# Kernel tuning notes

Measured on AMD Instinct MI355X. Metric: run time of the kernel, lower is better.

## Reference

```python
import jax, jax.numpy as jnp
import numpy as np

IMG_SIZE = 500
FM = 31
RATIOS = [1.0, 2.0, 0.5]
SCALES = [128, 256, 512]
PRE_NMS_TOPN = 6000
POST_NMS_TOPN = 1500
IOU_THRESHOLD = 0.7
VARIANCES = (0.1, 0.1, 0.2, 0.2)
BATCH = 64
TOTAL_ANCHORS = FM * FM * len(RATIOS) * len(SCALES)  # 8649


def generate_anchors():
    # normalized [y1, x1, y2, x2] anchors on a FM x FM grid
    stride = 1.0 / FM
    ctr = (np.arange(FM, dtype=np.float32) + 0.5) * stride
    cx, cy = np.meshgrid(ctr, ctr)
    centers = np.stack([cy.ravel(), cx.ravel()], axis=-1)  # [FM*FM, 2] (cy, cx)
    hs, ws = [], []
    for scale in SCALES:
        for ratio in RATIOS:
            ws.append((scale * np.sqrt(ratio)) / IMG_SIZE)
            hs.append((scale / np.sqrt(ratio)) / IMG_SIZE)
    hw = np.stack([np.array(hs, np.float32), np.array(ws, np.float32)], axis=-1)  # [9, 2]
    mins = centers[:, None, :] - hw[None] / 2.0
    maxs = centers[:, None, :] + hw[None] / 2.0
    boxes = np.concatenate([mins, maxs], axis=-1).reshape(-1, 4)  # [A, 4]
    return np.clip(boxes, 0.0, 1.0).astype(np.float32)


def delta_to_bbox(anchors, deltas):
    # anchors: [A,4], deltas: [B,A,4] (dy, dx, dh, dw) -> [B,A,4] (y1,x1,y2,x2)
    anc_h = anchors[:, 2] - anchors[:, 0]
    anc_w = anchors[:, 3] - anchors[:, 1]
    anc_cy = anchors[:, 0] + 0.5 * anc_h
    anc_cx = anchors[:, 1] + 0.5 * anc_w
    h = jnp.exp(deltas[..., 2]) * anc_h
    w = jnp.exp(deltas[..., 3]) * anc_w
    cy = deltas[..., 0] * anc_h + anc_cy
    cx = deltas[..., 1] * anc_w + anc_cx
    return jnp.stack([cy - 0.5 * h, cx - 0.5 * w, cy + 0.5 * h, cx + 0.5 * w], axis=-1)


def pairwise_iou_one_vs_all(sel_box, boxes):
    # sel_box: [B,1,4], boxes: [B,N,4] -> iou [B,N]
    y1 = jnp.maximum(sel_box[..., 0], boxes[..., 0])
    x1 = jnp.maximum(sel_box[..., 1], boxes[..., 1])
    y2 = jnp.minimum(sel_box[..., 2], boxes[..., 2])
    x2 = jnp.minimum(sel_box[..., 3], boxes[..., 3])
    inter = jnp.maximum(y2 - y1, 0.0) * jnp.maximum(x2 - x1, 0.0)
    area_s = (sel_box[..., 2] - sel_box[..., 0]) * (sel_box[..., 3] - sel_box[..., 1])
    area_b = (boxes[..., 2] - boxes[..., 0]) * (boxes[..., 3] - boxes[..., 1])
    return inter / (area_s + area_b - inter + 1e-9)


def batched_greedy_nms(boxes, scores, max_out, iou_threshold):
    # boxes [B,N,4], scores [B,N]; greedy NMS, vectorized over batch, scan over picks
    B, N, _ = boxes.shape

    def step(active, _):
        masked = jnp.where(active, scores, -jnp.inf)            # [B,N]
        idx = jnp.argmax(masked, axis=1)                         # [B]
        sel_score = jnp.take_along_axis(masked, idx[:, None], axis=1)[:, 0]
        sel_box = jnp.take_along_axis(boxes, idx[:, None, None], axis=1)  # [B,1,4]
        iou = pairwise_iou_one_vs_all(sel_box, boxes)            # [B,N]
        active = active & (iou <= iou_threshold)
        valid = jnp.isfinite(sel_score)
        out_box = jnp.where(valid[:, None], sel_box[:, 0, :], 0.0)
        out_score = jnp.where(valid, sel_score, 0.0)
        return active, (out_box, out_score)

    active0 = jnp.ones((B, N), dtype=bool)
    _, (out_boxes, out_scores) = jax.lax.scan(step, active0, None, length=max_out)
    out_boxes = jnp.transpose(out_boxes, (1, 0, 2))   # [B,max_out,4]
    out_scores = jnp.transpose(out_scores, (1, 0))    # [B,max_out]
    # tf.image.combined_non_max_suppression clips output boxes to [0,1] by default
    return jnp.clip(out_boxes, 0.0, 1.0), out_scores


def setup_inputs() -> dict:
    key = jax.random.key(0)
    k1, k2, k3 = jax.random.split(key, 3)
    rpn_bbox_deltas = jax.random.normal(k1, (BATCH, FM, FM, 36), dtype=jnp.float32)
    rpn_probs = jax.random.uniform(k2, (BATCH, FM, FM, 9), dtype=jnp.float32)
    gt_labels = jax.random.randint(k3, (BATCH, 10), 0, 20).astype(jnp.int64)
    anchors = jnp.asarray(generate_anchors())
    return {"rpn_bbox_deltas": rpn_bbox_deltas, "rpn_probs": rpn_probs,
            "gt_labels": gt_labels, "anchors": anchors}


def reference(rpn_bbox_deltas, rpn_probs, gt_labels, anchors):
    B = rpn_bbox_deltas.shape[0]
    A = anchors.shape[0]
    variances = jnp.asarray(VARIANCES, dtype=rpn_bbox_deltas.dtype)
    deltas = rpn_bbox_deltas.reshape(B, A, 4) * variances
    probs = rpn_probs.reshape(B, A)
    rpn_bboxes = delta_to_bbox(anchors, deltas)              # [B,A,4]
    top_scores, top_idx = jax.lax.top_k(probs, PRE_NMS_TOPN)  # sorted desc
    top_boxes = jnp.take_along_axis(rpn_bboxes, top_idx[:, :, None], axis=1)
    roi_bboxes, roi_scores = batched_greedy_nms(top_boxes, top_scores,
                                                POST_NMS_TOPN, IOU_THRESHOLD)
    return roi_bboxes, roi_scores
```

## Files before the change

kernel.cpp:

```cpp
#include <hip/hip_runtime.h>
#include <math.h>

typedef unsigned int u32;
typedef unsigned short u16;
typedef unsigned long long u64;

#define BATCH 64
#define A_TOT 8649
#define TOPN  6000
#define POST  1500
#define NB    4096
#define NT    512
#define NWAVE 8
#define NSLOT 12
#define NCHUNK 94
#define DONEBIT 0x80000000u
#define CNTMASK 0x7FFFFFFFu
#define GUARD_MAX (1 << 18)

#define LDS_BYTES 106496

__global__ __launch_bounds__(NT, 2) void roibbox_kernel(
    const float* __restrict__ deltas,
    const float* __restrict__ probs,
    const float* __restrict__ anchors,
    float* __restrict__ out)
{
    #pragma clang fp contract(off)
    __shared__ alignas(16) char smem[LDS_BYTES];
    u64*    keysL   = (u64*)   (smem + 0);
    u32*    bucketA = (u32*)   (smem + 69632);
    u32*    bucketB = (u32*)   (smem + 86016);
    u32*    stemp   = (u32*)   (smem + 102400);
    float4* ringL   = (float4*)(smem + 69632);
    u16*    ppL     = (u16*)   (smem + 93632);
    u32*    ctrlP   = (u32*)   (smem + 105632);
    u32*    ctrlF   = (u32*)   (smem + 105636);
    u32*    bmL     = (u32*)   (smem + 105640);

    const int tid = threadIdx.x;
    const int b   = blockIdx.x;
    const u32 lane = (u32)tid & 63u;
    const u32 w    = (u32)tid >> 6;
    const float* pb = probs + (size_t)b * A_TOT;

    #pragma unroll
    for (int i = 0; i < NB/NT; ++i) bucketA[tid + i*NT] = 0u;
    __syncthreads();

    for (int j = tid; j < A_TOT; j += NT) {
        float s = pb[j];
        int bkt = (int)(s * (float)NB);
        bkt = (NB-1) - min(max(bkt, 0), NB-1);
        atomicAdd(&bucketA[bkt], 1u);
    }
    __syncthreads();

    {
        int base8 = tid << 3;
        u32 c[8]; u32 ms = 0;
        #pragma unroll
        for (int i = 0; i < 8; ++i) { c[i] = bucketA[base8+i]; ms += c[i]; }
        stemp[tid] = ms;
        __syncthreads();
        int src = 0;
        for (int off = 1; off < NT; off <<= 1) {
            u32 v = stemp[src*NT + tid];
            if (tid >= off) v += stemp[src*NT + tid - off];
            stemp[(src^1)*NT + tid] = v;
            __syncthreads();
            src ^= 1;
        }
        u32 excl = stemp[src*NT + tid] - ms;
        #pragma unroll
        for (int i = 0; i < 8; ++i) {
            bucketA[base8+i] = excl; bucketB[base8+i] = excl; excl += c[i];
        }
    }
    __syncthreads();

    for (int j = tid; j < A_TOT; j += NT) {
        float s = pb[j];
        int bkt = (int)(s * (float)NB);
        bkt = (NB-1) - min(max(bkt, 0), NB-1);
        u32 pos = atomicAdd(&bucketB[bkt], 1u);
        keysL[pos] = ((u64)__float_as_uint(s) << 32) | (u64)(~(u32)j);
    }
    __syncthreads();

    for (int bkt = tid; bkt < NB; bkt += NT) {
        int begin = (int)bucketA[bkt], end = (int)bucketB[bkt];
        for (int k = begin + 1; k < end; ++k) {
            u64 key = keysL[k];
            int m = k - 1;
            while (m >= begin && keysL[m] < key) { keysL[m+1] = keysL[m]; --m; }
            keysL[m+1] = key;
        }
    }
    __syncthreads();

    float ry1[NSLOT], rx1[NSLOT], ry2[NSLOT], rx2[NSLOT], rA[NSLOT];
    u32 mask = 0;
    #pragma unroll
    for (int i = 0; i < NSLOT; ++i) {
        u32 s = (u32)i*8u + w;
        u32 r = s*64u + lane;
        ry1[i]=0.f; rx1[i]=0.f; ry2[i]=0.f; rx2[i]=0.f; rA[i]=0.f;
        if (s < NCHUNK && r < TOPN) {
            u64 k = keysL[r];
            u32 aidx = ~((u32)k);
            float4 av = *(const float4*)(anchors + (size_t)aidx * 4);
            float4 dv = *(const float4*)(deltas + ((size_t)b * A_TOT + aidx) * 4);
            float d0 = dv.x*0.1f, d1 = dv.y*0.1f, d2 = dv.z*0.2f, d3 = dv.w*0.2f;
            float ah = av.z - av.x, aw = av.w - av.y;
            float acy = av.x + 0.5f*ah, acx = av.y + 0.5f*aw;
            float h  = (float)exp((double)d2) * ah;
            float wd = (float)exp((double)d3) * aw;
            float cy = d0*ah + acy;
            float cx = d1*aw + acx;
            ry1[i] = cy - 0.5f*h;  rx1[i] = cx - 0.5f*wd;
            ry2[i] = cy + 0.5f*h;  rx2[i] = cx + 0.5f*wd;
            rA[i]  = (ry2[i]-ry1[i])*(rx2[i]-rx1[i]);
            mask |= 1u << i;
        }
    }
    u32 slotAlive = 0;
    #pragma unroll
    for (int i = 0; i < NSLOT; ++i)
        if (__ballot((mask >> i) & 1u)) slotAlive |= 1u << i;

    for (int j = tid; j < TOPN/2; j += NT) ((u32*)ppL)[j] = 0xFFFFFFFFu;
    if (tid == 0) { *ctrlP = 0u; *ctrlF = 0u; bmL[0] = 0u; bmL[1] = 0u; bmL[2] = 0xC0000000u; }
    __syncthreads();

    const double MTHR = (double)0.7f + 0x1p-25;

    auto scanNext = [&](u32 from) -> u32 {
        for (u32 k = from >> 5; k < 3u; ++k) {
            u32 v = ~__hip_atomic_load(&bmL[k], __ATOMIC_RELAXED, __HIP_MEMORY_SCOPE_WORKGROUP);
            if (k == (from >> 5)) v &= ~((1u << (from & 31u)) - 1u);
            if (v) return k*32u + (u32)__builtin_ctz(v);
        }
        return 96u;
    };

    u32 consumed = 0;
    for (int g = 0; g < GUARD_MAX; ++g) {
        u32 pv = __hip_atomic_load(ctrlP, __ATOMIC_ACQUIRE, __HIP_MEMORY_SCOPE_WORKGROUP);
        if (pv & DONEBIT) break;
        u32 cnt = pv & CNTMASK;

        if (cnt > consumed) {
            if (slotAlive) {
                float4 e = ringL[consumed];
                for (u32 q = consumed; q < cnt; ++q) {
                    float4 en = e;
                    if (q + 1 < cnt) en = ringL[q + 1];
                    float sA = (e.z - e.x) * (e.w - e.y);
                    #pragma unroll
                    for (int i = 0; i < NSLOT; ++i) {
                        if (slotAlive & (1u << i)) {
                            float yy1 = fmaxf(e.x, ry1[i]);
                            float xx1 = fmaxf(e.y, rx1[i]);
                            float yy2 = fminf(e.z, ry2[i]);
                            float xx2 = fminf(e.w, rx2[i]);
                            float inter = fmaxf(yy2 - yy1, 0.f) * fmaxf(xx2 - xx1, 0.f);
                            float den = ((sA + rA[i]) - inter) + 1e-9f;
                            if ((double)inter >= MTHR * (double)den) mask &= ~(1u << i);
                        }
                    }
                    e = en;
                }
                u32 na = 0;
                #pragma unroll
                for (int i = 0; i < NSLOT; ++i)
                    if ((slotAlive >> i) & 1u)
                        if (__ballot((mask >> i) & 1u)) na |= 1u << i;
                u32 died = slotAlive & ~na;
                slotAlive = na;
                if (died && lane == 0) {
                    #pragma unroll
                    for (int i = 0; i < NSLOT; ++i)
                        if ((died >> i) & 1u) {
                            u32 s = (u32)i*8u + w;
                            __hip_atomic_fetch_or(&bmL[s >> 5], 1u << (s & 31u),
                                                  __ATOMIC_RELAXED, __HIP_MEMORY_SCOPE_WORKGROUP);
                        }
                }
            }
            consumed = cnt;
            continue;
        }

        u32 f = __hip_atomic_load(ctrlF, __ATOMIC_ACQUIRE, __HIP_MEMORY_SCOPE_WORKGROUP);
        if ((f & 7u) == w) {
            u32 pv2 = __hip_atomic_load(ctrlP, __ATOMIC_ACQUIRE, __HIP_MEMORY_SCOPE_WORKGROUP);
            if (pv2 & DONEBIT) break;
            u32 cnt2 = pv2 & CNTMASK;
            if (cnt2 != consumed) continue;
            u32 fi = f >> 3;
            if ((slotAlive >> fi) & 1u) {
                float cy1, cx1, cy2, cx2, cA_;
                switch (fi) {
                    case 0:  cy1=ry1[0];  cx1=rx1[0];  cy2=ry2[0];  cx2=rx2[0];  cA_=rA[0];  break;
                    case 1:  cy1=ry1[1];  cx1=rx1[1];  cy2=ry2[1];  cx2=rx2[1];  cA_=rA[1];  break;
                    case 2:  cy1=ry1[2];  cx1=rx1[2];  cy2=ry2[2];  cx2=rx2[2];  cA_=rA[2];  break;
                    case 3:  cy1=ry1[3];  cx1=rx1[3];  cy2=ry2[3];  cx2=rx2[3];  cA_=rA[3];  break;
                    case 4:  cy1=ry1[4];  cx1=rx1[4];  cy2=ry2[4];  cx2=rx2[4];  cA_=rA[4];  break;
                    case 5:  cy1=ry1[5];  cx1=rx1[5];  cy2=ry2[5];  cx2=rx2[5];  cA_=rA[5];  break;
                    case 6:  cy1=ry1[6];  cx1=rx1[6];  cy2=ry2[6];  cx2=rx2[6];  cA_=rA[6];  break;
                    case 7:  cy1=ry1[7];  cx1=rx1[7];  cy2=ry2[7];  cx2=rx2[7];  cA_=rA[7];  break;
                    case 8:  cy1=ry1[8];  cx1=rx1[8];  cy2=ry2[8];  cx2=rx2[8];  cA_=rA[8];  break;
                    case 9:  cy1=ry1[9];  cx1=rx1[9];  cy2=ry2[9];  cx2=rx2[9];  cA_=rA[9];  break;
                    case 10: cy1=ry1[10]; cx1=rx1[10]; cy2=ry2[10]; cx2=rx2[10]; cA_=rA[10]; break;
                    default: cy1=ry1[11]; cx1=rx1[11]; cy2=ry2[11]; cx2=rx2[11]; cA_=rA[11]; break;
                }
                u64 am = __ballot((mask >> fi) & 1u);
                mask &= ~(1u << fi);
                slotAlive &= ~(1u << fi);
                u32 pc = cnt2;
                bool alldone = false;
                __builtin_amdgcn_s_setprio(1);
                while (true) {
                    if (!am) {
                        if (lane == 0)
                            __hip_atomic_fetch_or(&bmL[f >> 5], 1u << (f & 31u),
                                                  __ATOMIC_RELAXED, __HIP_MEMORY_SCOPE_WORKGROUP);
                        u32 nxt = scanNext(f + 1u);
                        if (nxt >= NCHUNK) {
                            if (lane == 0)
                                __hip_atomic_store(ctrlP, pc | DONEBIT, __ATOMIC_RELEASE,
                                                   __HIP_MEMORY_SCOPE_WORKGROUP);
                            alldone = true;
                        } else if (lane == 0) {
                            __hip_atomic_store(ctrlF, nxt, __ATOMIC_RELEASE,
                                               __HIP_MEMORY_SCOPE_WORKGROUP);
                        }
                        break;
                    }
                    u32 ol = (u32)__builtin_ctzll(am);
                    float sy1 = __uint_as_float((u32)__builtin_amdgcn_readlane((int)__float_as_uint(cy1), (int)ol));
                    float sx1 = __uint_as_float((u32)__builtin_amdgcn_readlane((int)__float_as_uint(cx1), (int)ol));
                    float sy2 = __uint_as_float((u32)__builtin_amdgcn_readlane((int)__float_as_uint(cy2), (int)ol));
                    float sx2 = __uint_as_float((u32)__builtin_amdgcn_readlane((int)__float_as_uint(cx2), (int)ol));
                    if (lane == ol) {
                        ppL[f*64u + ol] = (u16)pc;
                        ringL[pc] = make_float4(cy1, cx1, cy2, cx2);
                    }
                    float sA = (sy2 - sy1) * (sx2 - sx1);
                    float yy1 = fmaxf(sy1, cy1);
                    float xx1 = fmaxf(sx1, cx1);
                    float yy2 = fminf(sy2, cy2);
                    float xx2 = fminf(sx2, cx2);
                    float inter = fmaxf(yy2 - yy1, 0.f) * fmaxf(xx2 - xx1, 0.f);
                    float den = ((sA + cA_) - inter) + 1e-9f;
                    u64 supp = __ballot((double)inter >= MTHR * (double)den);
                    am &= ~supp;
                    ++pc;
                    u32 val = pc | ((pc >= POST) ? DONEBIT : 0u);
                    if (lane == 0)
                        __hip_atomic_store(ctrlP, val, __ATOMIC_RELEASE,
                                           __HIP_MEMORY_SCOPE_WORKGROUP);
                    if (pc >= POST) { alldone = true; break; }
                }
                __builtin_amdgcn_s_setprio(0);
                if (alldone) break;
                continue;
            } else {
                if (lane == 0)
                    __hip_atomic_fetch_or(&bmL[f >> 5], 1u << (f & 31u),
                                          __ATOMIC_RELAXED, __HIP_MEMORY_SCOPE_WORKGROUP);
                u32 nxt = scanNext(f + 1u);
                if (nxt >= NCHUNK) {
                    if (lane == 0)
                        __hip_atomic_store(ctrlP, cnt2 | DONEBIT, __ATOMIC_RELEASE,
                                           __HIP_MEMORY_SCOPE_WORKGROUP);
                    break;
                }
                if (lane == 0)
                    __hip_atomic_store(ctrlF, nxt, __ATOMIC_RELEASE,
                                       __HIP_MEMORY_SCOPE_WORKGROUP);
                continue;
            }
        }
        __builtin_amdgcn_s_sleep(1);
    }
    __syncthreads();
    u32 pend = (*ctrlP) & CNTMASK;

    const size_t sbase = (size_t)BATCH * POST * 4;
    #pragma unroll
    for (int i = 0; i < NSLOT; ++i) {
        u32 s = (u32)i*8u + w;
        u32 r = s*64u + lane;
        if (s < NCHUNK && r < TOPN) {
            u32 v = (u32)ppL[r];
            if (v != 0xFFFFu) {
                size_t row = (size_t)b * POST + v;
                float* ob = out + row * 4;
                ob[0] = fminf(fmaxf(ry1[i], 0.f), 1.f);
                ob[1] = fminf(fmaxf(rx1[i], 0.f), 1.f);
                ob[2] = fminf(fmaxf(ry2[i], 0.f), 1.f);
                ob[3] = fminf(fmaxf(rx2[i], 0.f), 1.f);
                out[sbase + row] = __uint_as_float((u32)(keysL[r] >> 32));
            }
        }
    }
    for (int p = (int)pend + tid; p < POST; p += NT) {
        size_t row = (size_t)b * POST + p;
        float* ob = out + row * 4;
        ob[0]=0.f; ob[1]=0.f; ob[2]=0.f; ob[3]=0.f;
        out[sbase + row] = 0.f;
    }
}

extern "C" void kernel_launch(void* const* d_in, const int* in_sizes, int n_in,
                              void* d_out, int out_size, void* d_ws, size_t ws_size,
                              hipStream_t stream) {
    const float* deltas  = (const float*)d_in[0];
    const float* probs   = (const float*)d_in[1];
    const float* anchors = (const float*)d_in[3];
    float* out = (float*)d_out;

    roibbox_kernel<<<dim3(BATCH), dim3(NT), 0, stream>>>(deltas, probs, anchors, out);
}
```

Before: 1.368 ms.

## Lazily apply suppression only to slots near the NMS frontier, with fp32 fast-path threshold

Each wave now tracks how far each register slot has been checked against the kept-box ring, and only applies new kept boxes to slots within a horizon of the current frontier chunk. Far-away slots catch up later, which lets them drop out early without testing every kept box, and avoids per-step IoU work on chunks that are still far from the frontier. The IoU comparison first uses fp32 bounds and falls back to the exact double check only when a lane is near the threshold. This adds bookkeeping and catch-up loops and makes the control flow more complex; the frontier wave must wait until its slot is fully caught up.

```diff
diff --git a/kernel.cpp b/kernel.cpp
--- a/kernel.cpp
+++ b/kernel.cpp
@@ -14,6 +14,7 @@
 #define NWAVE 8
 #define NSLOT 12
 #define NCHUNK 94
+#define HOR   12
 #define DONEBIT 0x80000000u
 #define CNTMASK 0x7FFFFFFFu
 #define GUARD_MAX (1 << 18)
@@ -129,6 +130,10 @@
     for (int i = 0; i < NSLOT; ++i)
         if (__ballot((mask >> i) & 1u)) slotAlive |= 1u << i;
 
+    u32 consS[NSLOT];
+    #pragma unroll
+    for (int i = 0; i < NSLOT; ++i) consS[i] = 0u;
+
     for (int j = tid; j < TOPN/2; j += NT) ((u32*)ppL)[j] = 0xFFFFFFFFu;
     if (tid == 0) { *ctrlP = 0u; *ctrlF = 0u; bmL[0] = 0u; bmL[1] = 0u; bmL[2] = 0xC0000000u; }
     __syncthreads();
@@ -144,62 +149,110 @@
         return 96u;
     };
 
-    u32 consumed = 0;
+    #define APPLY(i, e, sA)  do {                                              \
+        float yy1 = fmaxf((e).x, ry1[i]);                                      \
+        float xx1 = fmaxf((e).y, rx1[i]);                                      \
+        float yy2 = fminf((e).z, ry2[i]);                                      \
+        float xx2 = fminf((e).w, rx2[i]);                                      \
+        float inter = fmaxf(yy2 - yy1, 0.f) * fmaxf(xx2 - xx1, 0.f);           \
+        float den = (((sA) + rA[i]) - inter) + 1e-9f;     \
+        bool sup = inter >= 0.700001f * den;                                   \
+        bool amb = (!sup) && (inter >= 0.699999f * den);                       \
+        if (__any((int)amb)) sup = ((double)inter >= MTHR * (double)den);      \
+        if (sup) mask &= ~(1u << (i));                                         \
+    } while (0)
+
     for (int g = 0; g < GUARD_MAX; ++g) {
         u32 pv = __hip_atomic_load(ctrlP, __ATOMIC_ACQUIRE, __HIP_MEMORY_SCOPE_WORKGROUP);
         if (pv & DONEBIT) break;
-        u32 cnt = pv & CNTMASK;
-
-        if (cnt > consumed) {
-            if (slotAlive) {
-                float4 e = ringL[consumed];
-                for (u32 q = consumed; q < cnt; ++q) {
+        u32 cnt = (u32)__builtin_amdgcn_readfirstlane((int)(pv & CNTMASK));
+        u32 f = __hip_atomic_load(ctrlF, __ATOMIC_ACQUIRE, __HIP_MEMORY_SCOPE_WORKGROUP);
+        f = (u32)__builtin_amdgcn_readfirstlane((int)f);
+        bool did = false;
+
+        u32 hm = 0;
+        #pragma unroll
+        for (int i = 0; i < NSLOT; ++i) {
+            u32 s = (u32)i*8u + w;
+            if (((slotAlive >> i) & 1u) && s <= f + HOR) hm |= 1u << i;
+        }
+
+        if (hm) {
+            u32 cmax = 0;
+            #pragma unroll
+            for (int i = 0; i < NSLOT; ++i)
+                if ((hm >> i) & 1u) cmax = max(cmax, consS[i]);
+            #pragma unroll
+            for (int i = 0; i < NSLOT; ++i) {
+                if (((hm >> i) & 1u) && consS[i] < cmax) {
+                    for (u32 q = consS[i]; q < cmax; ++q) {
+                        float4 e = ringL[q];
+                        float sA = (e.z - e.x) * (e.w - e.y);
+                        APPLY(i, e, sA);
+                    }
+                    consS[i] = cmax;
+                    did = true;
+                }
+            }
+            if (cmax < cnt) {
+                float4 e = ringL[cmax];
+                for (u32 q = cmax; q < cnt; ++q) {
                     float4 en = e;
                     if (q + 1 < cnt) en = ringL[q + 1];
                     float sA = (e.z - e.x) * (e.w - e.y);
                     #pragma unroll
-                    for (int i = 0; i < NSLOT; ++i) {
-                        if (slotAlive & (1u << i)) {
-                            float yy1 = fmaxf(e.x, ry1[i]);
-                            float xx1 = fmaxf(e.y, rx1[i]);
-                            float yy2 = fminf(e.z, ry2[i]);
-                            float xx2 = fminf(e.w, rx2[i]);
-                            float inter = fmaxf(yy2 - yy1, 0.f) * fmaxf(xx2 - xx1, 0.f);
-                            float den = ((sA + rA[i]) - inter) + 1e-9f;
-                            if ((double)inter >= MTHR * (double)den) mask &= ~(1u << i);
-                        }
-                    }
+                    for (int i = 0; i < NSLOT; ++i)
+                        if ((hm >> i) & 1u) APPLY(i, e, sA);
                     e = en;
                 }
-                u32 na = 0;
                 #pragma unroll
                 for (int i = 0; i < NSLOT; ++i)
-                    if ((slotAlive >> i) & 1u)
-                        if (__ballot((mask >> i) & 1u)) na |= 1u << i;
-                u32 died = slotAlive & ~na;
+                    if ((hm >> i) & 1u) consS[i] = cnt;
+                did = true;
+            }
+            if (did) {
+                u32 na = slotAlive;
+                #pragma unroll
+                for (int i = 0; i < NSLOT; ++i)
+                    if ((hm >> i) & 1u)
+                        if (!__ballot((mask >> i) & 1u)) na &= ~(1u << i);
+                u32 diedm = slotAlive & ~na;
                 slotAlive = na;
-                if (died && lane == 0) {
+                if (diedm && lane == 0) {
                     #pragma unroll
                     for (int i = 0; i < NSLOT; ++i)
-                        if ((died >> i) & 1u) {
+                        if ((diedm >> i) & 1u) {
                             u32 s = (u32)i*8u + w;
                             __hip_atomic_fetch_or(&bmL[s >> 5], 1u << (s & 31u),
                                                   __ATOMIC_RELAXED, __HIP_MEMORY_SCOPE_WORKGROUP);
                         }
                 }
             }
-            consumed = cnt;
-            continue;
-        }
-
-        u32 f = __hip_atomic_load(ctrlF, __ATOMIC_ACQUIRE, __HIP_MEMORY_SCOPE_WORKGROUP);
-        if ((f & 7u) == w) {
+        }
+
+        if ((f & 7u) == w && f < NCHUNK) {
             u32 pv2 = __hip_atomic_load(ctrlP, __ATOMIC_ACQUIRE, __HIP_MEMORY_SCOPE_WORKGROUP);
             if (pv2 & DONEBIT) break;
             u32 cnt2 = pv2 & CNTMASK;
-            if (cnt2 != consumed) continue;
+            if (cnt2 != cnt) continue;
             u32 fi = f >> 3;
+            u32 cfi;
+            switch (fi) {
+                case 0:  cfi = consS[0];  break;
+                case 1:  cfi = consS[1];  break;
+                case 2:  cfi = consS[2];  break;
+                case 3:  cfi = consS[3];  break;
+                case 4:  cfi = consS[4];  break;
+                case 5:  cfi = consS[5];  break;
+                case 6:  cfi = consS[6];  break;
+                case 7:  cfi = consS[7];  break;
+                case 8:  cfi = consS[8];  break;
+                case 9:  cfi = consS[9];  break;
+                case 10: cfi = consS[10]; break;
+                default: cfi = consS[11]; break;
+            }
             if ((slotAlive >> fi) & 1u) {
+                if (cfi != cnt2) continue;
                 float cy1, cx1, cy2, cx2, cA_;
                 switch (fi) {
                     case 0:  cy1=ry1[0];  cx1=rx1[0];  cy2=ry2[0];  cx2=rx2[0];  cA_=rA[0];  break;
@@ -283,7 +336,7 @@
                 continue;
             }
         }
-        __builtin_amdgcn_s_sleep(1);
+        if (!did) __builtin_amdgcn_s_sleep(1);
     }
     __syncthreads();
     u32 pend = (*ctrlP) & CNTMASK;
@@ -312,6 +365,7 @@
         ob[0]=0.f; ob[1]=0.f; ob[2]=0.f; ob[3]=0.f;
         out[sbase + row] = 0.f;
     }
+    #undef APPLY
 }
 
 extern "C" void kernel_launch(void* const* d_in, const int* in_sizes, int n_in,
```

Result: slower. 2.265 ms (+65.6%).

## Lazily admit NMS slots into a horizon window with incremental catch-up

Applied to the files above, without the earlier changes.

Instead of testing every alive slot against every newly kept box, each wave now tracks only a 'hot' set of slots near the current frontier (within a horizon). Slots beyond the horizon are brought in later by replaying the kept-box ring incrementally, a bounded number of entries per idle iteration. The aim is to cut the per-kept-box IoU work spread over all 12 slots and keep waves doing useful catch-up while idle. The cost is extra control complexity, forced catch-up on the critical path when the frontier reaches a slot that has not been replayed yet, and possible scheduling stalls.

```diff
diff --git a/kernel.cpp b/kernel.cpp
--- a/kernel.cpp
+++ b/kernel.cpp
@@ -14,6 +14,8 @@
 #define NWAVE 8
 #define NSLOT 12
 #define NCHUNK 94
+#define HOR   16u
+#define ENTSTEP 64u
 #define DONEBIT 0x80000000u
 #define CNTMASK 0x7FFFFFFFu
 #define GUARD_MAX (1 << 18)
@@ -124,10 +126,6 @@
             mask |= 1u << i;
         }
     }
-    u32 slotAlive = 0;
-    #pragma unroll
-    for (int i = 0; i < NSLOT; ++i)
-        if (__ballot((mask >> i) & 1u)) slotAlive |= 1u << i;
 
     for (int j = tid; j < TOPN/2; j += NT) ((u32*)ppL)[j] = 0xFFFFFFFFu;
     if (tid == 0) { *ctrlP = 0u; *ctrlF = 0u; bmL[0] = 0u; bmL[1] = 0u; bmL[2] = 0xC0000000u; }
@@ -144,62 +142,119 @@
         return 96u;
     };
 
+    #define APPLY(i, e, sA)  do {                                              \
+        float yy1 = fmaxf((e).x, ry1[i]);                                      \
+        float xx1 = fmaxf((e).y, rx1[i]);                                      \
+        float yy2 = fminf((e).z, ry2[i]);                                      \
+        float xx2 = fminf((e).w, rx2[i]);                                      \
+        float inter = fmaxf(yy2 - yy1, 0.f) * fmaxf(xx2 - xx1, 0.f);           \
+        float den = (((sA) + rA[i]) - inter) + 1e-9f;     \
+        if ((double)inter >= MTHR * (double)den) mask &= ~(1u << (i));         \
+    } while (0)
+
+    #define ENTRUN(I, tgt) do {                                                \
+        u32 q_ = entC;                                                         \
+        if (q_ < (tgt)) {                                                      \
+            float4 e0_ = ringL[q_];                                            \
+            float4 e1_ = (q_+1 < (tgt)) ? ringL[q_+1] : e0_;                   \
+            for (; q_ < (tgt); ++q_) {                                         \
+                float4 e_ = e0_; e0_ = e1_;                                    \
+                if (q_+2 < (tgt)) e1_ = ringL[q_+2];                           \
+                float sA_ = (e_.z - e_.x) * (e_.w - e_.y);                     \
+                APPLY(I, e_, sA_);                                             \
+            }                                                                  \
+            entC = (tgt);                                                      \
+        }                                                                      \
+    } while (0)
+
+    u32 hmask = 0;
     u32 consumed = 0;
+    u32 hnext = 0;
+    u32 entSlot = NSLOT;
+    u32 entC = 0;
+
+    auto ent_step = [&](u32 tgt) {
+        switch (entSlot) {
+            case 0:  ENTRUN(0,  tgt); break;
+            case 1:  ENTRUN(1,  tgt); break;
+            case 2:  ENTRUN(2,  tgt); break;
+            case 3:  ENTRUN(3,  tgt); break;
+            case 4:  ENTRUN(4,  tgt); break;
+            case 5:  ENTRUN(5,  tgt); break;
+            case 6:  ENTRUN(6,  tgt); break;
+            case 7:  ENTRUN(7,  tgt); break;
+            case 8:  ENTRUN(8,  tgt); break;
+            case 9:  ENTRUN(9,  tgt); break;
+            case 10: ENTRUN(10, tgt); break;
+            default: ENTRUN(11, tgt); break;
+        }
+    };
+    auto ent_promote = [&]() {
+        u32 es = entSlot;
+        if (__ballot((mask >> es) & 1u)) hmask |= 1u << es;
+        else if (lane == 0) {
+            u32 s = es*8u + w;
+            __hip_atomic_fetch_or(&bmL[s >> 5], 1u << (s & 31u),
+                                  __ATOMIC_RELAXED, __HIP_MEMORY_SCOPE_WORKGROUP);
+        }
+        entSlot = NSLOT;
+    };
+    auto group_consume = [&](u32 cnt) {
+        if (consumed >= cnt) return;
+        if (hmask) {
+            u32 q = consumed;
+            float4 e0 = ringL[q];
+            float4 e1 = (q+1 < cnt) ? ringL[q+1] : e0;
+            for (; q < cnt; ++q) {
+                float4 e = e0; e0 = e1;
+                if (q+2 < cnt) e1 = ringL[q+2];
+                float sA = (e.z - e.x) * (e.w - e.y);
+                #pragma unroll
+                for (int i = 0; i < NSLOT; ++i)
+                    if ((hmask >> i) & 1u) APPLY(i, e, sA);
+            }
+            u32 nh = hmask;
+            #pragma unroll
+            for (int i = 0; i < NSLOT; ++i)
+                if ((hmask >> i) & 1u)
+                    if (!__ballot((mask >> i) & 1u)) nh &= ~(1u << i);
+            u32 diedm = hmask & ~nh;
+            hmask = nh;
+            if (diedm && lane == 0) {
+                #pragma unroll
+                for (int i = 0; i < NSLOT; ++i)
+                    if ((diedm >> i) & 1u) {
+                        u32 s = (u32)i*8u + w;
+                        __hip_atomic_fetch_or(&bmL[s >> 5], 1u << (s & 31u),
+                                              __ATOMIC_RELAXED, __HIP_MEMORY_SCOPE_WORKGROUP);
+                    }
+            }
+        }
+        consumed = cnt;
+    };
+
     for (int g = 0; g < GUARD_MAX; ++g) {
         u32 pv = __hip_atomic_load(ctrlP, __ATOMIC_ACQUIRE, __HIP_MEMORY_SCOPE_WORKGROUP);
         if (pv & DONEBIT) break;
         u32 cnt = pv & CNTMASK;
-
-        if (cnt > consumed) {
-            if (slotAlive) {
-                float4 e = ringL[consumed];
-                for (u32 q = consumed; q < cnt; ++q) {
-                    float4 en = e;
-                    if (q + 1 < cnt) en = ringL[q + 1];
-                    float sA = (e.z - e.x) * (e.w - e.y);
-                    #pragma unroll
-                    for (int i = 0; i < NSLOT; ++i) {
-                        if (slotAlive & (1u << i)) {
-                            float yy1 = fmaxf(e.x, ry1[i]);
-                            float xx1 = fmaxf(e.y, rx1[i]);
-                            float yy2 = fminf(e.z, ry2[i]);
-                            float xx2 = fminf(e.w, rx2[i]);
-                            float inter = fmaxf(yy2 - yy1, 0.f) * fmaxf(xx2 - xx1, 0.f);
-                            float den = ((sA + rA[i]) - inter) + 1e-9f;
-                            if ((double)inter >= MTHR * (double)den) mask &= ~(1u << i);
-                        }
-                    }
-                    e = en;
-                }
-                u32 na = 0;
-                #pragma unroll
-                for (int i = 0; i < NSLOT; ++i)
-                    if ((slotAlive >> i) & 1u)
-                        if (__ballot((mask >> i) & 1u)) na |= 1u << i;
-                u32 died = slotAlive & ~na;
-                slotAlive = na;
-                if (died && lane == 0) {
-                    #pragma unroll
-                    for (int i = 0; i < NSLOT; ++i)
-                        if ((died >> i) & 1u) {
-                            u32 s = (u32)i*8u + w;
-                            __hip_atomic_fetch_or(&bmL[s >> 5], 1u << (s & 31u),
-                                                  __ATOMIC_RELAXED, __HIP_MEMORY_SCOPE_WORKGROUP);
-                        }
-                }
-            }
-            consumed = cnt;
-            continue;
-        }
-
         u32 f = __hip_atomic_load(ctrlF, __ATOMIC_ACQUIRE, __HIP_MEMORY_SCOPE_WORKGROUP);
-        if ((f & 7u) == w) {
+
+        if ((f & 7u) == w && f < NCHUNK) {
             u32 pv2 = __hip_atomic_load(ctrlP, __ATOMIC_ACQUIRE, __HIP_MEMORY_SCOPE_WORKGROUP);
             if (pv2 & DONEBIT) break;
             u32 cnt2 = pv2 & CNTMASK;
-            if (cnt2 != consumed) continue;
+            group_consume(cnt2);
             u32 fi = f >> 3;
-            if ((slotAlive >> fi) & 1u) {
+            if (entSlot < NSLOT && entSlot <= fi) { ent_step(consumed); ent_promote(); }
+            if (hnext <= fi) {
+                u32 svS = entSlot, svC = entC;
+                while (hnext <= fi) {
+                    entSlot = hnext++; entC = 0;
+                    ent_step(consumed); ent_promote();
+                }
+                entSlot = svS; entC = svC;
+            }
+            if ((hmask >> fi) & 1u) {
                 float cy1, cx1, cy2, cx2, cA_;
                 switch (fi) {
                     case 0:  cy1=ry1[0];  cx1=rx1[0];  cy2=ry2[0];  cx2=rx2[0];  cA_=rA[0];  break;
@@ -217,7 +272,7 @@
                 }
                 u64 am = __ballot((mask >> fi) & 1u);
                 mask &= ~(1u << fi);
-                slotAlive &= ~(1u << fi);
+                hmask &= ~(1u << fi);
                 u32 pc = cnt2;
                 bool alldone = false;
                 __builtin_amdgcn_s_setprio(1);
@@ -267,9 +322,6 @@
                 if (alldone) break;
                 continue;
             } else {
-                if (lane == 0)
-                    __hip_atomic_fetch_or(&bmL[f >> 5], 1u << (f & 31u),
-                                          __ATOMIC_RELAXED, __HIP_MEMORY_SCOPE_WORKGROUP);
                 u32 nxt = scanNext(f + 1u);
                 if (nxt >= NCHUNK) {
                     if (lane == 0)
@@ -283,7 +335,27 @@
                 continue;
             }
         }
-        __builtin_amdgcn_s_sleep(1);
+
+        bool idle = true;
+        if (cnt > consumed) { group_consume(cnt); idle = false; }
+        if (entSlot < NSLOT) {
+            if (entC < consumed) {
+                u32 tgt = consumed; u32 lim = entC + ENTSTEP;
+                if (lim < tgt) tgt = lim;
+                ent_step(tgt);
+                idle = false;
+            }
+            if (entC == consumed) ent_promote();
+        } else if (hnext < NSLOT) {
+            u32 s = (u32)hnext*8u + w;
+            if (s >= NCHUNK) hnext = NSLOT;
+            else if (s <= f + HOR) {
+                entSlot = hnext++; entC = 0;
+                if (entC == consumed) ent_promote();
+                idle = false;
+            }
+        }
+        if (idle) __builtin_amdgcn_s_sleep(2);
     }
     __syncthreads();
     u32 pend = (*ctrlP) & CNTMASK;
@@ -312,6 +384,8 @@
         ob[0]=0.f; ob[1]=0.f; ob[2]=0.f; ob[3]=0.f;
         out[sbase + row] = 0.f;
     }
+    #undef APPLY
+    #undef ENTRUN
 }
 
 extern "C" void kernel_launch(void* const* d_in, const int* in_sizes, int n_in,
```

Result: faster. 1.269 ms (-7.2%).

## Batch ring consumption with fast float IoU filter and throttle progress publishing

Applied to the files above, without the earlier changes.

Consumer waves now process published keepers in groups of four using a float-only IoU test with a narrow ambiguity band. They fall back to the exact double comparison only when some lane lands near the threshold. The owner wave publishes its progress counter every four keepers instead of every one. It also consumes outstanding keepers itself before becoming owner instead of spinning, and idle waves back off with increasing sleep. This aims to cut double-precision math, LDS atomic traffic and polling contention in the serial NMS loop, at the cost of more complex synchronisation and consumers lagging behind the owner.

```diff
diff --git a/kernel.cpp b/kernel.cpp
--- a/kernel.cpp
+++ b/kernel.cpp
@@ -124,10 +124,10 @@
             mask |= 1u << i;
         }
     }
-    u32 slotAlive = 0;
+    u32 hmask = 0;
     #pragma unroll
     for (int i = 0; i < NSLOT; ++i)
-        if (__ballot((mask >> i) & 1u)) slotAlive |= 1u << i;
+        if (__ballot((mask >> i) & 1u)) hmask |= 1u << i;
 
     for (int j = tid; j < TOPN/2; j += NT) ((u32*)ppL)[j] = 0xFFFFFFFFu;
     if (tid == 0) { *ctrlP = 0u; *ctrlF = 0u; bmL[0] = 0u; bmL[1] = 0u; bmL[2] = 0xC0000000u; }
@@ -144,62 +144,105 @@
         return 96u;
     };
 
+    #define APF(i, e, sA, amb) do {                                            \
+        float yy1 = fmaxf((e).x, ry1[i]);                                      \
+        float xx1 = fmaxf((e).y, rx1[i]);                                      \
+        float yy2 = fminf((e).z, ry2[i]);                                      \
+        float xx2 = fminf((e).w, rx2[i]);                                      \
+        float inter = fmaxf(yy2 - yy1, 0.f) * fmaxf(xx2 - xx1, 0.f);           \
+        float den = (((sA) + rA[i]) - inter) + 1e-9f;     \
+        if (inter >= 0.700004f * den) mask &= ~(1u << (i));                    \
+        else if (inter >= 0.699996f * den) (amb) = 1u;                         \
+    } while (0)
+
+    #define APX(i, e, sA) do {                                                 \
+        float yy1 = fmaxf((e).x, ry1[i]);                                      \
+        float xx1 = fmaxf((e).y, rx1[i]);                                      \
+        float yy2 = fminf((e).z, ry2[i]);                                      \
+        float xx2 = fminf((e).w, rx2[i]);                                      \
+        float inter = fmaxf(yy2 - yy1, 0.f) * fmaxf(xx2 - xx1, 0.f);           \
+        float den = (((sA) + rA[i]) - inter) + 1e-9f;                          \
+        if ((double)inter >= MTHR * (double)den) mask &= ~(1u << (i));         \
+    } while (0)
+
     u32 consumed = 0;
+
+    auto group_consume = [&](u32 cnt) {
+        if (consumed >= cnt) return;
+        if (!hmask) { consumed = cnt; return; }
+        u32 q = consumed;
+        u32 n = cnt - q; if (n > 4u) n = 4u;
+        float4 p0 = ringL[q];
+        float4 p1 = (n > 1u) ? ringL[q+1] : p0;
+        float4 p2 = (n > 2u) ? ringL[q+2] : p0;
+        float4 p3 = (n > 3u) ? ringL[q+3] : p0;
+        while (true) {
+            float4 e0 = p0, e1 = p1, e2 = p2, e3 = p3;
+            u32 bn = n;
+            u32 nq = q + bn;
+            if (nq < cnt) {
+                n = cnt - nq; if (n > 4u) n = 4u;
+                p0 = ringL[nq];
+                p1 = (n > 1u) ? ringL[nq+1] : p0;
+                p2 = (n > 2u) ? ringL[nq+2] : p0;
+                p3 = (n > 3u) ? ringL[nq+3] : p0;
+            }
+            float a0 = (e0.z - e0.x) * (e0.w - e0.y);
+            float a1 = (e1.z - e1.x) * (e1.w - e1.y);
+            float a2 = (e2.z - e2.x) * (e2.w - e2.y);
+            float a3 = (e3.z - e3.x) * (e3.w - e3.y);
+            #pragma unroll
+            for (int i = 0; i < NSLOT; ++i) {
+                if ((hmask >> i) & 1u) {
+                    u32 amb = 0u;
+                    APF(i, e0, a0, amb);
+                    if (bn > 1u) APF(i, e1, a1, amb);
+                    if (bn > 2u) APF(i, e2, a2, amb);
+                    if (bn > 3u) APF(i, e3, a3, amb);
+                    if (__any((int)amb)) {
+                        APX(i, e0, a0);
+                        if (bn > 1u) APX(i, e1, a1);
+                        if (bn > 2u) APX(i, e2, a2);
+                        if (bn > 3u) APX(i, e3, a3);
+                    }
+                }
+            }
+            q = nq;
+            if (q >= cnt) break;
+        }
+        u32 nh = hmask;
+        #pragma unroll
+        for (int i = 0; i < NSLOT; ++i)
+            if ((hmask >> i) & 1u)
+                if (!__ballot((mask >> i) & 1u)) nh &= ~(1u << i);
+        u32 diedm = hmask & ~nh;
+        hmask = nh;
+        if (diedm && lane == 0) {
+            #pragma unroll
+            for (int i = 0; i < NSLOT; ++i)
+                if ((diedm >> i) & 1u) {
+                    u32 s = (u32)i*8u + w;
+                    __hip_atomic_fetch_or(&bmL[s >> 5], 1u << (s & 31u),
+                                          __ATOMIC_RELAXED, __HIP_MEMORY_SCOPE_WORKGROUP);
+                }
+        }
+        consumed = cnt;
+    };
+
+    u32 lastCnt = 0xFFFFFFFFu, lastF = 0xFFFFFFFFu, bk = 0;
     for (int g = 0; g < GUARD_MAX; ++g) {
         u32 pv = __hip_atomic_load(ctrlP, __ATOMIC_ACQUIRE, __HIP_MEMORY_SCOPE_WORKGROUP);
         if (pv & DONEBIT) break;
         u32 cnt = pv & CNTMASK;
-
-        if (cnt > consumed) {
-            if (slotAlive) {
-                float4 e = ringL[consumed];
-                for (u32 q = consumed; q < cnt; ++q) {
-                    float4 en = e;
-                    if (q + 1 < cnt) en = ringL[q + 1];
-                    float sA = (e.z - e.x) * (e.w - e.y);
-                    #pragma unroll
-                    for (int i = 0; i < NSLOT; ++i) {
-                        if (slotAlive & (1u << i)) {
-                            float yy1 = fmaxf(e.x, ry1[i]);
-                            float xx1 = fmaxf(e.y, rx1[i]);
-                            float yy2 = fminf(e.z, ry2[i]);
-                            float xx2 = fminf(e.w, rx2[i]);
-                            float inter = fmaxf(yy2 - yy1, 0.f) * fmaxf(xx2 - xx1, 0.f);
-                            float den = ((sA + rA[i]) - inter) + 1e-9f;
-                            if ((double)inter >= MTHR * (double)den) mask &= ~(1u << i);
-                        }
-                    }
-                    e = en;
-                }
-                u32 na = 0;
-                #pragma unroll
-                for (int i = 0; i < NSLOT; ++i)
-                    if ((slotAlive >> i) & 1u)
-                        if (__ballot((mask >> i) & 1u)) na |= 1u << i;
-                u32 died = slotAlive & ~na;
-                slotAlive = na;
-                if (died && lane == 0) {
-                    #pragma unroll
-                    for (int i = 0; i < NSLOT; ++i)
-                        if ((died >> i) & 1u) {
-                            u32 s = (u32)i*8u + w;
-                            __hip_atomic_fetch_or(&bmL[s >> 5], 1u << (s & 31u),
-                                                  __ATOMIC_RELAXED, __HIP_MEMORY_SCOPE_WORKGROUP);
-                        }
-                }
-            }
-            consumed = cnt;
-            continue;
-        }
-
         u32 f = __hip_atomic_load(ctrlF, __ATOMIC_ACQUIRE, __HIP_MEMORY_SCOPE_WORKGROUP);
-        if ((f & 7u) == w) {
+
+        if ((f & 7u) == w && f < NCHUNK) {
             u32 pv2 = __hip_atomic_load(ctrlP, __ATOMIC_ACQUIRE, __HIP_MEMORY_SCOPE_WORKGROUP);
             if (pv2 & DONEBIT) break;
             u32 cnt2 = pv2 & CNTMASK;
-            if (cnt2 != consumed) continue;
+            group_consume(cnt2);
             u32 fi = f >> 3;
-            if ((slotAlive >> fi) & 1u) {
+            if ((hmask >> fi) & 1u) {
                 float cy1, cx1, cy2, cx2, cA_;
                 switch (fi) {
                     case 0:  cy1=ry1[0];  cx1=rx1[0];  cy2=ry2[0];  cx2=rx2[0];  cA_=rA[0];  break;
@@ -217,15 +260,18 @@
                 }
                 u64 am = __ballot((mask >> fi) & 1u);
                 mask &= ~(1u << fi);
-                slotAlive &= ~(1u << fi);
+                hmask &= ~(1u << fi);
                 u32 pc = cnt2;
                 bool alldone = false;
                 __builtin_amdgcn_s_setprio(1);
                 while (true) {
                     if (!am) {
-                        if (lane == 0)
+                        if (lane == 0) {
+                            __hip_atomic_store(ctrlP, pc, __ATOMIC_RELEASE,
+                                               __HIP_MEMORY_SCOPE_WORKGROUP);
                             __hip_atomic_fetch_or(&bmL[f >> 5], 1u << (f & 31u),
                                                   __ATOMIC_RELAXED, __HIP_MEMORY_SCOPE_WORKGROUP);
+                        }
                         u32 nxt = scanNext(f + 1u);
                         if (nxt >= NCHUNK) {
                             if (lane == 0)
@@ -257,19 +303,21 @@
                     u64 supp = __ballot((double)inter >= MTHR * (double)den);
                     am &= ~supp;
                     ++pc;
-                    u32 val = pc | ((pc >= POST) ? DONEBIT : 0u);
-                    if (lane == 0)
-                        __hip_atomic_store(ctrlP, val, __ATOMIC_RELEASE,
+                    if (pc >= POST) {
+                        if (lane == 0)
+                            __hip_atomic_store(ctrlP, pc | DONEBIT, __ATOMIC_RELEASE,
+                                               __HIP_MEMORY_SCOPE_WORKGROUP);
+                        alldone = true; break;
+                    }
+                    if ((pc & 3u) == 0u && lane == 0)
+                        __hip_atomic_store(ctrlP, pc, __ATOMIC_RELEASE,
                                            __HIP_MEMORY_SCOPE_WORKGROUP);
-                    if (pc >= POST) { alldone = true; break; }
                 }
                 __builtin_amdgcn_s_setprio(0);
                 if (alldone) break;
+                lastCnt = 0xFFFFFFFFu; bk = 0;
                 continue;
             } else {
-                if (lane == 0)
-                    __hip_atomic_fetch_or(&bmL[f >> 5], 1u << (f & 31u),
-                                          __ATOMIC_RELAXED, __HIP_MEMORY_SCOPE_WORKGROUP);
                 u32 nxt = scanNext(f + 1u);
                 if (nxt >= NCHUNK) {
                     if (lane == 0)
@@ -280,10 +328,23 @@
                 if (lane == 0)
                     __hip_atomic_store(ctrlF, nxt, __ATOMIC_RELEASE,
                                        __HIP_MEMORY_SCOPE_WORKGROUP);
+                bk = 0;
                 continue;
             }
         }
-        __builtin_amdgcn_s_sleep(1);
+
+        bool work = false;
+        if (cnt > consumed) { group_consume(cnt); work = true; }
+        if (!work && cnt == lastCnt && f == lastF) {
+            if      (bk == 0) __builtin_amdgcn_s_sleep(1);
+            else if (bk == 1) __builtin_amdgcn_s_sleep(2);
+            else if (bk == 2) __builtin_amdgcn_s_sleep(4);
+            else              __builtin_amdgcn_s_sleep(8);
+            if (bk < 3) ++bk;
+        } else {
+            bk = 0;
+        }
+        lastCnt = cnt; lastF = f;
     }
     __syncthreads();
     u32 pend = (*ctrlP) & CNTMASK;
@@ -312,6 +373,8 @@
         ob[0]=0.f; ob[1]=0.f; ob[2]=0.f; ob[3]=0.f;
         out[sbase + row] = 0.f;
     }
+    #undef APF
+    #undef APX
 }
 
 extern "C" void kernel_launch(void* const* d_in, const int* in_sizes, int n_in,
```

Result: slower. 1.795 ms (+31.2%).
